# Kernel tuning notes

Measured on AMD Instinct MI355X. Metric: run time of the kernel, lower is better.

Reference implementation:

```python
import jax, jax.numpy as jnp
import numpy as np
from jax import lax

D_MODEL = 128
D_INNER = 256   # expand * d_model
D_STATE = 16
D_CONV = 4
DT_RANK = 8     # ceil(d_model / 16)
IN_CH = 64
SCALE = 0.02


def setup_inputs() -> dict:
    key = jax.random.key(0)
    ks = jax.random.split(key, 16)
    r = lambda k, s: jax.random.normal(k, s, dtype=jnp.float32)
    return {
        "x": r(ks[0], (4, IN_CH, 128, 128)),
        "conv_w": r(ks[1], (D_MODEL, IN_CH, 3, 3)) * SCALE,
        "conv_b": r(ks[2], (D_MODEL,)) * SCALE,
        "bn_g": jnp.ones((D_MODEL,), jnp.float32),
        "bn_b": jnp.zeros((D_MODEL,), jnp.float32),
        "bn_mean": r(ks[3], (D_MODEL,)) * SCALE,
        "bn_var": jax.random.uniform(ks[4], (D_MODEL,), jnp.float32) + 0.5,
        "in_w": r(ks[5], (2 * D_INNER, D_MODEL)) * SCALE,
        "conv1d_w": r(ks[6], (D_INNER, 1, D_CONV)) * SCALE,
        "conv1d_b": r(ks[7], (D_INNER,)) * SCALE,
        "xproj_w": r(ks[8], (DT_RANK + 2 * D_STATE, D_INNER)) * SCALE,
        "dtproj_w": r(ks[9], (D_INNER, DT_RANK)) * SCALE,
        "dtproj_b": r(ks[10], (D_INNER,)) * SCALE,
        "A_log": r(ks[11], (D_INNER, D_STATE)) * 0.5,
        "Dp": r(ks[12], (D_INNER,)) * SCALE,
        "out_w": r(ks[13], (D_MODEL, D_INNER)) * SCALE,
    }


def _mamba(u, in_w, conv1d_w, conv1d_b, xproj_w, dtproj_w, dtproj_b, A_log, Dp, out_w):
    # u: [B, L, d_model]
    xz = jnp.einsum("bld,ed->ble", u, in_w)          # [B, L, 2*d_inner]
    x_in, z = jnp.split(xz, 2, axis=-1)
    # depthwise causal conv1d over L
    xc = lax.conv_general_dilated(
        x_in.transpose(0, 2, 1), conv1d_w, (1,), [(D_CONV - 1, 0)],
        dimension_numbers=("NCL", "OIL", "NCL"), feature_group_count=D_INNER,
    ) + conv1d_b[None, :, None]
    x_in = jax.nn.silu(xc).transpose(0, 2, 1)         # [B, L, d_inner]

    x_dbl = jnp.einsum("bld,ed->ble", x_in, xproj_w)  # [B, L, dt_rank+2*d_state]
    dt, Bm, Cm = jnp.split(x_dbl, [DT_RANK, DT_RANK + D_STATE], axis=-1)
    delta = jax.nn.softplus(jnp.einsum("blr,dr->bld", dt, dtproj_w) + dtproj_b)

    A = -jnp.exp(A_log)                               # [d_inner, d_state]
    deltaA = jnp.exp(jnp.einsum("bld,dn->bldn", delta, A))        # [B,L,d,n]
    deltaBu = jnp.einsum("bld,bln,bld->bldn", delta, Bm, x_in)    # [B,L,d,n]

    def step(h, inp):
        dA, dBu, c = inp                              # [B,d,n],[B,d,n],[B,n]
        h = dA * h + dBu
        y = jnp.einsum("bdn,bn->bd", h, c)
        return h, y

    Bsz, L = u.shape[0], u.shape[1]
    h0 = jnp.zeros((Bsz, D_INNER, D_STATE), u.dtype)
    _, ys = lax.scan(step, h0, (deltaA.transpose(1, 0, 2, 3),
                                deltaBu.transpose(1, 0, 2, 3),
                                Cm.transpose(1, 0, 2)))
    y = ys.transpose(1, 0, 2) + x_in * Dp             # [B, L, d_inner]
    y = y * jax.nn.silu(z)
    return jnp.einsum("bld,ed->ble", y, out_w)        # [B, L, d_model]


def reference(x, conv_w, conv_b, bn_g, bn_b, bn_mean, bn_var, in_w, conv1d_w,
              conv1d_b, xproj_w, dtproj_w, dtproj_b, A_log, Dp, out_w):
    # downsample: conv3x3 stride2 + BN(eval) + exact GELU
    y = lax.conv_general_dilated(x, conv_w, (2, 2), [(1, 1), (1, 1)],
                                 dimension_numbers=("NCHW", "OIHW", "NCHW"))
    y = y + conv_b[None, :, None, None]
    inv = bn_g / jnp.sqrt(bn_var + 1e-5)
    y = (y - bn_mean[None, :, None, None]) * inv[None, :, None, None] + bn_b[None, :, None, None]
    y = jax.nn.gelu(y, approximate=False)             # [B, C, H, W]

    B, C, H, W = y.shape
    u = y.reshape(B, C, H * W).transpose(0, 2, 1)     # [B, L, C]
    out = _mamba(u, in_w, conv1d_w, conv1d_b, xproj_w, dtproj_w, dtproj_b,
                 A_log, Dp, out_w)
    out = out.transpose(0, 2, 1).reshape(B, C, H, W)
    return y + out
```

## Files before the change

### kernel.cpp

```cpp
#include <hip/hip_runtime.h>
#include <math.h>

#define NB 4
#define LTOK 4096
#define DM 128
#define DI 256
#define NCH 256
#define TCH 16
#define GSZ 16
#define NG  16

#define OFF_A2     0u
#define OFF_BIAS2  73728u
#define OFF_YDSR   84096u
#define OFF_XPRE   2181248u
#define OFF_Z      6375552u
#define OFF_DELTA  10569856u
#define OFF_YABF   12667008u
#define OFF_BC     14764160u
#define OFF_DSUM   15288448u
#define OFF_GS     15550592u
#define OFF_GD     15812736u
#define OFF_XT     15829120u
#define OFF_WBF    17926272u
#define OFF_WCMP   17963136u
#define OFF_YDSBF  18004096u
#define OFF_INWBF  19052672u
#define OFF_OUTWBF 19085440u

#define DEV __device__ __forceinline__
#define L2E 1.4426950408889634f

typedef short bh8 __attribute__((ext_vector_type(8)));
typedef float f4v __attribute__((ext_vector_type(4)));

DEV float fast_silu(float v) {
  return v * __builtin_amdgcn_rcpf(1.f + __expf(-v));
}

DEV unsigned short f2bf(float f) {
  unsigned int u = __float_as_uint(f);
  u = (u + 0x7FFFu + ((u >> 16) & 1u)) >> 16;
  return (unsigned short)u;
}

DEV float bf2f(unsigned short us) {
  return __uint_as_float((unsigned int)us << 16);
}

__global__ __launch_bounds__(256) void k0_prep(
    const float* __restrict__ conv_w, const float* __restrict__ conv_b,
    const float* __restrict__ bn_g, const float* __restrict__ bn_b,
    const float* __restrict__ bn_mean, const float* __restrict__ bn_var,
    const float* __restrict__ xproj_w, const float* __restrict__ A_log,
    const float* __restrict__ dtw, const float* __restrict__ in_w,
    const float* __restrict__ out_w, float* __restrict__ ws) {
  int i = blockIdx.x * 256 + threadIdx.x;
  if (i < 73728) {
    int ci = i & 63; int tap = (i >> 6) % 9; int co = i / 576;
    float inv = bn_g[co] * rsqrtf(bn_var[co] + 1e-5f);
    ((unsigned short*)(ws + OFF_WBF))[i] = f2bf(conv_w[co * 576 + ci * 9 + tap] * inv);
  } else if (i < 73856) {
    int co = i - 73728;
    float inv = bn_g[co] * rsqrtf(bn_var[co] + 1e-5f);
    ws[OFF_BIAS2 + co] = (conv_b[co] - bn_mean[co]) * inv + bn_b[co];
  } else if (i < 77952) {
    int j = i - 73856;
    ws[OFF_A2 + j] = -__expf(A_log[j]) * L2E;
  } else if (i < 159872) {
    int j = i - 77952;
    int n = j >> 8, k = j & 255;
    float v = 0.f;
    if (n < 256) {
#pragma unroll
      for (int r = 0; r < 8; ++r)
        v = fmaf(dtw[n * 8 + r], xproj_w[r * 256 + k], v);
    } else if (n < 288) {
      v = xproj_w[(8 + n - 256) * 256 + k];
    }
    ((unsigned short*)(ws + OFF_WCMP))[j] = f2bf(v);
  } else if (i < 225408) {
    int j = i - 159872;
    ((unsigned short*)(ws + OFF_INWBF))[j] = f2bf(in_w[j]);
  } else if (i < 258176) {
    int j = i - 225408;
    ((unsigned short*)(ws + OFF_OUTWBF))[j] = f2bf(out_w[j]);
  }
}

__global__ __launch_bounds__(256) void k0b_transpose(
    const float* __restrict__ x, unsigned short* __restrict__ xt) {
  __shared__ float t[64][65];
  const int tid = threadIdx.x;
  const int ixh = blockIdx.x & 1;
  const int iy = (blockIdx.x >> 1) & 127;
  const int b = blockIdx.x >> 8;
  {
    const int ixl = tid & 63, cw = tid >> 6;
#pragma unroll 4
    for (int i = 0; i < 16; ++i) {
      int ci = cw * 16 + i;
      t[ci][ixl] = x[(((size_t)(b * 64 + ci) * 128) + iy) * 128 + ixh * 64 + ixl];
    }
  }
  __syncthreads();
  {
    const int cil = tid & 63, iw = tid >> 6;
    unsigned short* dst = xt + (((size_t)(b * 128 + iy) * 128) + ixh * 64) * 64;
#pragma unroll 4
    for (int i = 0; i < 16; ++i) {
      int ix = iw * 16 + i;
      dst[ix * 64 + cil] = f2bf(t[cil][ix]);
    }
  }
}

__global__ __launch_bounds__(256) void k1_conv_mfma(
    const unsigned short* __restrict__ xt, const unsigned short* __restrict__ wbf,
    const float* __restrict__ bias2, unsigned short* __restrict__ ydsr,
    unsigned short* __restrict__ ydsbf) {
  __shared__ unsigned short ldt[64][66];
  const int tid = threadIdx.x;
  const int lane = tid & 63;
  const int w = tid >> 6;
  const int col = lane & 15, quad = lane >> 4;
  const int cohalf = blockIdx.x & 1;
  const int oy = (blockIdx.x >> 1) & 63;
  const int b = blockIdx.x >> 7;
  const int co0 = cohalf * 64 + (w & 1) * 32;
  const int tok0 = (w >> 1) * 32;
  const int iy0 = 2 * oy - 1;
  const bh8 bzero = {};
  f4v acc[2][2];
#pragma unroll
  for (int mt = 0; mt < 2; ++mt)
#pragma unroll
    for (int nt = 0; nt < 2; ++nt) acc[mt][nt] = (f4v){0.f, 0.f, 0.f, 0.f};

  const unsigned short* ap0 = wbf + (size_t)(co0 + col) * 576;
  const unsigned short* ap1 = wbf + (size_t)(co0 + 16 + col) * 576;

  for (int tap = 0; tap < 9; ++tap) {
    const int kh = tap / 3, kw = tap - kh * 3;
    const int iy = iy0 + kh;
    const int ix0 = 2 * (tok0 + col) - 1 + kw;
    const int ix1 = ix0 + 32;
    const unsigned short* xrow = xt + (long)(b * 128 + iy) * 8192;
    const bool ok0 = (iy >= 0) && (ix0 >= 0);
    const bool ok1 = (iy >= 0);
#pragma unroll
    for (int kc = 0; kc < 2; ++kc) {
      const int cib = kc * 32 + quad * 8;
      bh8 a0 = *(const bh8*)&ap0[tap * 64 + cib];
      bh8 a1 = *(const bh8*)&ap1[tap * 64 + cib];
      bh8 b0 = *(const bh8*)&xrow[(long)ix0 * 64 + cib];
      bh8 b1 = *(const bh8*)&xrow[(long)ix1 * 64 + cib];
      if (!ok0) b0 = bzero;
      if (!ok1) b1 = bzero;
      acc[0][0] = __builtin_amdgcn_mfma_f32_16x16x32_bf16(a0, b0, acc[0][0], 0, 0, 0);
      acc[1][0] = __builtin_amdgcn_mfma_f32_16x16x32_bf16(a1, b0, acc[1][0], 0, 0, 0);
      acc[0][1] = __builtin_amdgcn_mfma_f32_16x16x32_bf16(a0, b1, acc[0][1], 0, 0, 0);
      acc[1][1] = __builtin_amdgcn_mfma_f32_16x16x32_bf16(a1, b1, acc[1][1], 0, 0, 0);
    }
  }
#pragma unroll
  for (int mt = 0; mt < 2; ++mt)
#pragma unroll
    for (int nt = 0; nt < 2; ++nt) {
      const int tok = tok0 + nt * 16 + col;
#pragma unroll
      for (int r = 0; r < 4; ++r) {
        const int co = co0 + mt * 16 + quad * 4 + r;
        float v = acc[mt][nt][r] + bias2[co];
        float g = 0.5f * v * (1.f + erff(v * 0.70710678118f));
        unsigned short gb = f2bf(g);
        ydsr[(((size_t)(b * 128 + co) * 64) + oy) * 64 + tok] = gb;
        ldt[tok][(w & 1) * 32 + mt * 16 + quad * 4 + r] = gb;
      }
    }
  __syncthreads();
  {
    const int tok = tid >> 2, cg = (tid & 3) * 16;
    unsigned short* dst =
        ydsbf + ((size_t)(b * 4096 + oy * 64 + tok)) * 128 + cohalf * 64 + cg;
#pragma unroll
    for (int j = 0; j < 8; ++j)
      ((unsigned int*)dst)[j] = *(const unsigned int*)&ldt[tok][cg + 2 * j];
  }
}

__global__ __launch_bounds__(256) void k2_mfma(
    const unsigned short* __restrict__ ydsbf, const unsigned short* __restrict__ inwbf,
    unsigned short* __restrict__ xpre, unsigned short* __restrict__ z) {
  const int tid = threadIdx.x;
  const int lane = tid & 63;
  const int w = tid >> 6;
  const int col = lane & 15, quad = lane >> 4;
  const int tt = blockIdx.x & 255, b = blockIdx.x >> 8;
  const int t0 = tt * 16;
  bh8 afrag[4];
  {
    const unsigned short* arow = ydsbf + (size_t)(b * 4096 + t0 + col) * 128 + quad * 8;
#pragma unroll
    for (int kb = 0; kb < 4; ++kb) afrag[kb] = *(const bh8*)&arow[kb * 32];
  }
  f4v acc[8];
#pragma unroll
  for (int j = 0; j < 8; ++j) acc[j] = (f4v){0.f, 0.f, 0.f, 0.f};
  const int nt0 = w * 8;
  const unsigned short* wb = inwbf + (size_t)(nt0 * 16 + col) * 128 + quad * 8;
#pragma unroll
  for (int kb = 0; kb < 4; ++kb) {
#pragma unroll
    for (int j = 0; j < 8; ++j) {
      bh8 bfrag = *(const bh8*)&wb[(size_t)j * 2048 + kb * 32];
      acc[j] = __builtin_amdgcn_mfma_f32_16x16x32_bf16(afrag[kb], bfrag, acc[j], 0, 0, 0);
    }
  }
#pragma unroll
  for (int j = 0; j < 8; ++j) {
    const int e = (nt0 + j) * 16 + col;
#pragma unroll
    for (int r = 0; r < 4; ++r) {
      const int t = t0 + quad * 4 + r;
      if (e < 256) xpre[((size_t)(b * 4096 + t)) * 256 + e] = f2bf(acc[j][r]);
      else z[((size_t)(b * 4096 + t)) * 256 + e - 256] = f2bf(acc[j][r]);
    }
  }
}

__global__ __launch_bounds__(256) void k4_mfma(
    const unsigned short* __restrict__ wcomp, const float* __restrict__ dtb,
    const unsigned short* __restrict__ xpre, const float* __restrict__ cw1,
    const float* __restrict__ cb1, unsigned short* __restrict__ xinbf,
    unsigned short* __restrict__ delta, float* __restrict__ bc,
    float* __restrict__ dsum) {
  __shared__ unsigned short ld_xin[16][264];
  __shared__ unsigned short ld_delta[16][264];
  __shared__ float ld_bc[16][33];
  const int tid = threadIdx.x;
  const int lane = tid & 63;
  const int w = tid >> 6;
  const int col = lane & 15, quad = lane >> 4;
  const int tt = blockIdx.x & 255, b = blockIdx.x >> 8;
  const int t0 = tt * 16;

  {
    const int d = tid;
    float4 w4 = *(const float4*)&cw1[d * 4];
    float bias = cb1[d];
    float xw[19];
#pragma unroll
    for (int i = 0; i < 19; ++i) {
      int t = t0 - 3 + i;
      xw[i] = (t >= 0) ? bf2f(xpre[((size_t)(b * 4096 + t)) * 256 + d]) : 0.f;
    }
    unsigned short* dst = xinbf + ((size_t)(b * 4096 + t0)) * 256 + d;
#pragma unroll
    for (int i = 0; i < 16; ++i) {
      float o = bias + w4.x * xw[i] + w4.y * xw[i + 1] + w4.z * xw[i + 2] +
                w4.w * xw[i + 3];
      unsigned short us = f2bf(fast_silu(o));
      ld_xin[i][d] = us;
      dst[(size_t)i * 256] = us;
    }
  }
  __syncthreads();

  bh8 afrag[8];
#pragma unroll
  for (int kb = 0; kb < 8; ++kb)
    afrag[kb] = *(const bh8*)&ld_xin[col][quad * 8 + kb * 32];
  f4v acc[5];
#pragma unroll
  for (int j = 0; j < 5; ++j) acc[j] = (f4v){0.f, 0.f, 0.f, 0.f};

  const int nt0 = w * 5;
  const unsigned short* wb = wcomp + (size_t)(nt0 * 16 + col) * 256 + quad * 8;
#pragma unroll
  for (int kb = 0; kb < 8; ++kb) {
#pragma unroll
    for (int j = 0; j < 5; ++j) {
      bh8 bfrag = *(const bh8*)&wb[(size_t)j * 4096 + kb * 32];
      acc[j] = __builtin_amdgcn_mfma_f32_16x16x32_bf16(afrag[kb], bfrag, acc[j], 0, 0, 0);
    }
  }
#pragma unroll
  for (int j = 0; j < 5; ++j) {
    const int n = (nt0 + j) * 16 + col;
    if (n < 256) {
      float bias = dtb[n];
#pragma unroll
      for (int r = 0; r < 4; ++r) {
        float s = acc[j][r] + bias;
        float dl = fmaxf(s, 0.f) + __logf(1.f + __expf(-fabsf(s)));
        ld_delta[quad * 4 + r][n] = f2bf(dl);
      }
    } else if (n < 288) {
#pragma unroll
      for (int r = 0; r < 4; ++r) ld_bc[quad * 4 + r][n - 256] = acc[j][r];
    }
  }
  __syncthreads();

  {
    float ds = 0.f;
#pragma unroll
    for (int i = 0; i < 16; ++i) ds += bf2f(ld_delta[i][tid]);
    dsum[((size_t)b * 256 + tt) * 256 + tid] = ds;
  }
#pragma unroll
  for (int it = 0; it < 4; ++it) {
    int idx = it * 256 + tid;
    int row = idx >> 6, d4 = (idx & 63) * 4;
    unsigned long long pk = *(const unsigned long long*)&ld_delta[row][d4];
    *(unsigned long long*)&delta[((size_t)(b * 4096 + t0 + row)) * 256 + d4] = pk;
  }
  if (tid < 128) {
    int row = tid >> 3, q = (tid & 7) * 4;
    float4 v = make_float4(ld_bc[row][q], ld_bc[row][q + 1],
                           ld_bc[row][q + 2], ld_bc[row][q + 3]);
    *(float4*)&bc[((size_t)(b * 4096 + t0 + row)) * 32 + q] = v;
  }
}

__global__ __launch_bounds__(256) void k5a_scan1(
    const unsigned short* __restrict__ xinbf, const float* __restrict__ bc,
    const unsigned short* __restrict__ delta, const float* __restrict__ a2tab,
    float* __restrict__ S) {
  __shared__ __align__(16) float bct[TCH * 32];
  const int tid = threadIdx.x;
  const int d = tid;
  const int c = blockIdx.x & (NCH - 1), b = blockIdx.x >> 8;
  const int t0 = c * TCH;
  {
    const float* src = bc + (size_t)(b * 4096 + t0) * 32;
    for (int i = tid; i < TCH * 32; i += 256) bct[i] = src[i];
  }
  float A2[16];
#pragma unroll
  for (int j = 0; j < 4; ++j) {
    float4 a = *(const float4*)&a2tab[d * 16 + j * 4];
    A2[4 * j + 0] = a.x; A2[4 * j + 1] = a.y; A2[4 * j + 2] = a.z; A2[4 * j + 3] = a.w;
  }
  float h[16];
#pragma unroll
  for (int n = 0; n < 16; ++n) h[n] = 0.f;
  const unsigned short* pd = delta + (size_t)(b * 4096 + t0) * 256 + d;
  const unsigned short* px = xinbf + (size_t)(b * 4096 + t0) * 256 + d;
  __syncthreads();
#pragma unroll 4
  for (int i = 0; i < TCH; ++i) {
    float dl = bf2f(pd[(size_t)i * 256]);
    float xv = bf2f(px[(size_t)i * 256]);
    float dlx = dl * xv;
    const float* r = &bct[i * 32];
    float4 B0 = *(const float4*)&r[0];
    float4 B1 = *(const float4*)&r[4];
    float4 B2 = *(const float4*)&r[8];
    float4 B3 = *(const float4*)&r[12];
    float Bv[16] = {B0.x, B0.y, B0.z, B0.w, B1.x, B1.y, B1.z, B1.w,
                    B2.x, B2.y, B2.z, B2.w, B3.x, B3.y, B3.z, B3.w};
#pragma unroll
    for (int n = 0; n < 16; ++n)
      h[n] = fmaf(exp2f(dl * A2[n]), h[n], dlx * Bv[n]);
  }
  const size_t sbase = ((size_t)(b * NCH + c) * 16) * 256 + d;
#pragma unroll
  for (int n = 0; n < 16; ++n) S[sbase + (size_t)n * 256] = h[n];
}

__global__ __launch_bounds__(256) void k5b1_group(
    float* __restrict__ S, const float* __restrict__ dsum,
    const float* __restrict__ a2tab, float* __restrict__ Gs,
    float* __restrict__ Gd) {
  const int d = threadIdx.x;
  const int n = blockIdx.x & 15, g = (blockIdx.x >> 4) & (NG - 1),
            b = blockIdx.x >> 8;
  const float A2 = a2tab[d * 16 + n];
  float h = 0.f, cum = 0.f;
#pragma unroll 4
  for (int c16 = 0; c16 < GSZ; ++c16) {
    int c = g * GSZ + c16;
    size_t si = ((size_t)(b * NCH + c) * 16 + n) * 256 + d;
    float s = S[si];
    float dsv = dsum[((size_t)b * NCH + c) * 256 + d];
    float P = exp2f(A2 * dsv);
    S[si] = h;
    h = fmaf(P, h, s);
    cum += dsv;
  }
  Gs[((size_t)(b * NG + g) * 16 + n) * 256 + d] = h;
  if (n == 0) Gd[((size_t)b * NG + g) * 256 + d] = cum;
}

__global__ __launch_bounds__(256) void k5b2_groupscan(
    float* __restrict__ Gs, const float* __restrict__ Gd,
    const float* __restrict__ a2tab) {
  const int d = threadIdx.x;
  const int n = blockIdx.x & 15, b = blockIdx.x >> 4;
  const float A2 = a2tab[d * 16 + n];
  float h = 0.f;
#pragma unroll
  for (int g = 0; g < NG; ++g) {
    size_t gi = ((size_t)(b * NG + g) * 16 + n) * 256 + d;
    float s = Gs[gi];
    float P = exp2f(A2 * Gd[((size_t)b * NG + g) * 256 + d]);
    Gs[gi] = h;
    h = fmaf(P, h, s);
  }
}

__global__ __launch_bounds__(256) void k5c_scan2(
    const unsigned short* __restrict__ xinbf, const float* __restrict__ bc,
    const unsigned short* __restrict__ delta, const unsigned short* __restrict__ z,
    const float* __restrict__ a2tab, const float* __restrict__ Dp,
    const float* __restrict__ dsum, const float* __restrict__ Gs,
    const float* __restrict__ S, unsigned short* __restrict__ yabf) {
  __shared__ __align__(16) float bct[TCH * 32];
  const int tid = threadIdx.x;
  const int d = tid;
  const int c = blockIdx.x & (NCH - 1), b = blockIdx.x >> 8;
  const int t0 = c * TCH;
  {
    const float* src = bc + (size_t)(b * 4096 + t0) * 32;
    for (int i = tid; i < TCH * 32; i += 256) bct[i] = src[i];
  }
  float A2[16];
#pragma unroll
  for (int j = 0; j < 4; ++j) {
    float4 a = *(const float4*)&a2tab[d * 16 + j * 4];
    A2[4 * j + 0] = a.x; A2[4 * j + 1] = a.y; A2[4 * j + 2] = a.z; A2[4 * j + 3] = a.w;
  }
  const float Dpd = Dp[d];
  const int g = c >> 4, c16 = c & 15;
  float dpref = 0.f;
  {
    const float* pds = dsum + ((size_t)b * NCH + g * GSZ) * 256 + d;
    for (int cc = 0; cc < c16; ++cc) dpref += pds[(size_t)cc * 256];
  }
  const size_t sbase = ((size_t)(b * NCH + c) * 16) * 256 + d;
  const size_t gbase = ((size_t)(b * NG + g) * 16) * 256 + d;
  float h[16];
#pragma unroll
  for (int n = 0; n < 16; ++n) {
    float gi = Gs[gbase + (size_t)n * 256];
    float hl = S[sbase + (size_t)n * 256];
    h[n] = fmaf(exp2f(A2[n] * dpref), gi, hl);
  }
  const size_t base = (size_t)(b * 4096 + t0) * 256 + d;
  const unsigned short* pd = delta + base;
  const unsigned short* px = xinbf + base;
  const unsigned short* pz = z + base;
  unsigned short* py = yabf + base;
  __syncthreads();
#pragma unroll 4
  for (int i = 0; i < TCH; ++i) {
    float dl = bf2f(pd[(size_t)i * 256]);
    float xv = bf2f(px[(size_t)i * 256]);
    float zv = bf2f(pz[(size_t)i * 256]);
    float dlx = dl * xv;
    const float* r = &bct[i * 32];
    float4 B0 = *(const float4*)&r[0];
    float4 B1 = *(const float4*)&r[4];
    float4 B2 = *(const float4*)&r[8];
    float4 B3 = *(const float4*)&r[12];
    float4 C0 = *(const float4*)&r[16];
    float4 C1 = *(const float4*)&r[20];
    float4 C2 = *(const float4*)&r[24];
    float4 C3 = *(const float4*)&r[28];
    float Bv[16] = {B0.x, B0.y, B0.z, B0.w, B1.x, B1.y, B1.z, B1.w,
                    B2.x, B2.y, B2.z, B2.w, B3.x, B3.y, B3.z, B3.w};
    float Cv[16] = {C0.x, C0.y, C0.z, C0.w, C1.x, C1.y, C1.z, C1.w,
                    C2.x, C2.y, C2.z, C2.w, C3.x, C3.y, C3.z, C3.w};
    float y = 0.f;
#pragma unroll
    for (int n = 0; n < 16; ++n) {
      h[n] = fmaf(exp2f(dl * A2[n]), h[n], dlx * Bv[n]);
      y = fmaf(h[n], Cv[n], y);
    }
    py[(size_t)i * 256] = f2bf((y + xv * Dpd) * fast_silu(zv));
  }
}

__global__ __launch_bounds__(256) void k6_mfma(
    const unsigned short* __restrict__ yabf, const unsigned short* __restrict__ outwbf,
    const unsigned short* __restrict__ ydsr, float* __restrict__ out) {
  __shared__ float ld[16][132];
  const int tid = threadIdx.x;
  const int lane = tid & 63;
  const int w = tid >> 6;
  const int col = lane & 15, quad = lane >> 4;
  const int tt = blockIdx.x & 255, b = blockIdx.x >> 8;
  const int t0 = tt * 16;
  const int oy = t0 >> 6, ox0 = t0 & 63;
  bh8 afrag[8];
  {
    const unsigned short* arow = yabf + (size_t)(b * 4096 + t0 + col) * 256 + quad * 8;
#pragma unroll
    for (int kb = 0; kb < 8; ++kb) afrag[kb] = *(const bh8*)&arow[kb * 32];
  }
  f4v acc[2];
#pragma unroll
  for (int j = 0; j < 2; ++j) acc[j] = (f4v){0.f, 0.f, 0.f, 0.f};
  const int nt0 = w * 2;
  const unsigned short* wb = outwbf + (size_t)(nt0 * 16 + col) * 256 + quad * 8;
#pragma unroll
  for (int kb = 0; kb < 8; ++kb) {
#pragma unroll
    for (int j = 0; j < 2; ++j) {
      bh8 bfrag = *(const bh8*)&wb[(size_t)j * 4096 + kb * 32];
      acc[j] = __builtin_amdgcn_mfma_f32_16x16x32_bf16(afrag[kb], bfrag, acc[j], 0, 0, 0);
    }
  }
#pragma unroll
  for (int j = 0; j < 2; ++j)
#pragma unroll
    for (int r = 0; r < 4; ++r)
      ld[quad * 4 + r][(nt0 + j) * 16 + col] = acc[j][r];
  __syncthreads();
  {
    const int cc = tid >> 1, half = tid & 1;
    size_t base = (((size_t)(b * 128 + cc) * 64) + oy) * 64 + ox0 + half * 8;
    const unsigned short* rp = ydsr + base;
    const int m0 = half * 8;
    float4 o0 = make_float4(ld[m0 + 0][cc] + bf2f(rp[0]), ld[m0 + 1][cc] + bf2f(rp[1]),
                            ld[m0 + 2][cc] + bf2f(rp[2]), ld[m0 + 3][cc] + bf2f(rp[3]));
    float4 o1 = make_float4(ld[m0 + 4][cc] + bf2f(rp[4]), ld[m0 + 5][cc] + bf2f(rp[5]),
                            ld[m0 + 6][cc] + bf2f(rp[6]), ld[m0 + 7][cc] + bf2f(rp[7]));
    *(float4*)&out[base] = o0;
    *(float4*)&out[base + 4] = o1;
  }
}

extern "C" void kernel_launch(void* const* d_in, const int* in_sizes, int n_in,
                              void* d_out, int out_size, void* d_ws, size_t ws_size,
                              hipStream_t stream) {
  (void)in_sizes; (void)n_in; (void)out_size; (void)ws_size;
  const float* x        = (const float*)d_in[0];
  const float* conv_w   = (const float*)d_in[1];
  const float* conv_b   = (const float*)d_in[2];
  const float* bn_g     = (const float*)d_in[3];
  const float* bn_b     = (const float*)d_in[4];
  const float* bn_mean  = (const float*)d_in[5];
  const float* bn_var   = (const float*)d_in[6];
  const float* in_w     = (const float*)d_in[7];
  const float* conv1d_w = (const float*)d_in[8];
  const float* conv1d_b = (const float*)d_in[9];
  const float* xproj_w  = (const float*)d_in[10];
  const float* dtproj_w = (const float*)d_in[11];
  const float* dtproj_b = (const float*)d_in[12];
  const float* A_log    = (const float*)d_in[13];
  const float* Dp       = (const float*)d_in[14];
  const float* out_w    = (const float*)d_in[15];
  float* ws = (float*)d_ws;
  float* out = (float*)d_out;

  k0_prep<<<1009, 256, 0, stream>>>(conv_w, conv_b, bn_g, bn_b, bn_mean, bn_var,
                                    xproj_w, A_log, dtproj_w, in_w, out_w, ws);
  k0b_transpose<<<1024, 256, 0, stream>>>(x, (unsigned short*)(ws + OFF_XT));
  k1_conv_mfma<<<512, 256, 0, stream>>>((const unsigned short*)(ws + OFF_XT),
                                        (const unsigned short*)(ws + OFF_WBF),
                                        ws + OFF_BIAS2,
                                        (unsigned short*)(ws + OFF_YDSR),
                                        (unsigned short*)(ws + OFF_YDSBF));
  k2_mfma<<<1024, 256, 0, stream>>>((const unsigned short*)(ws + OFF_YDSBF),
                                    (const unsigned short*)(ws + OFF_INWBF),
                                    (unsigned short*)(ws + OFF_XPRE),
                                    (unsigned short*)(ws + OFF_Z));
  k4_mfma<<<1024, 256, 0, stream>>>((const unsigned short*)(ws + OFF_WCMP),
                                    dtproj_b,
                                    (const unsigned short*)(ws + OFF_XPRE),
                                    conv1d_w, conv1d_b,
                                    (unsigned short*)(ws + OFF_XT),
                                    (unsigned short*)(ws + OFF_DELTA),
                                    ws + OFF_BC, ws + OFF_DSUM);
  k5a_scan1<<<1024, 256, 0, stream>>>((const unsigned short*)(ws + OFF_XT),
                                      ws + OFF_BC,
                                      (const unsigned short*)(ws + OFF_DELTA),
                                      ws + OFF_A2, ws + OFF_XPRE);
  k5b1_group<<<1024, 256, 0, stream>>>(ws + OFF_XPRE, ws + OFF_DSUM, ws + OFF_A2,
                                       ws + OFF_GS, ws + OFF_GD);
  k5b2_groupscan<<<64, 256, 0, stream>>>(ws + OFF_GS, ws + OFF_GD, ws + OFF_A2);
  k5c_scan2<<<1024, 256, 0, stream>>>((const unsigned short*)(ws + OFF_XT),
                                      ws + OFF_BC,
                                      (const unsigned short*)(ws + OFF_DELTA),
                                      (const unsigned short*)(ws + OFF_Z),
                                      ws + OFF_A2, Dp, ws + OFF_DSUM,
                                      ws + OFF_GS, ws + OFF_XPRE,
                                      (unsigned short*)(ws + OFF_YABF));
  k6_mfma<<<1024, 256, 0, stream>>>((const unsigned short*)(ws + OFF_YABF),
                                    (const unsigned short*)(ws + OFF_OUTWBF),
                                    (const unsigned short*)(ws + OFF_YDSR), out);
}
```

Before: 240.9 us.

## Fuse chunked scan phases into one cooperative kernel with grid syncs

```diff
diff --git a/kernel.cpp b/kernel.cpp
--- a/kernel.cpp
+++ b/kernel.cpp
@@ -1,5 +1,8 @@
 #include <hip/hip_runtime.h>
+#include <hip/hip_cooperative_groups.h>
 #include <math.h>
+
+namespace cg = cooperative_groups;
 
 #define NB 4
 #define LTOK 4096
@@ -27,6 +30,7 @@
 #define OFF_YDSBF  18004096u
 #define OFF_INWBF  19052672u
 #define OFF_OUTWBF 19085440u
+#define OFF_DPREF  19101824u
 
 #define DEV __device__ __forceinline__
 #define L2E 1.4426950408889634f
@@ -48,14 +52,42 @@
   return __uint_as_float((unsigned int)us << 16);
 }
 
-__global__ __launch_bounds__(256) void k0_prep(
-    const float* __restrict__ conv_w, const float* __restrict__ conv_b,
-    const float* __restrict__ bn_g, const float* __restrict__ bn_b,
-    const float* __restrict__ bn_mean, const float* __restrict__ bn_var,
-    const float* __restrict__ xproj_w, const float* __restrict__ A_log,
-    const float* __restrict__ dtw, const float* __restrict__ in_w,
-    const float* __restrict__ out_w, float* __restrict__ ws) {
-  int i = blockIdx.x * 256 + threadIdx.x;
+__global__ __launch_bounds__(256) void k0_all(
+    const float* __restrict__ x, const float* __restrict__ conv_w,
+    const float* __restrict__ conv_b, const float* __restrict__ bn_g,
+    const float* __restrict__ bn_b, const float* __restrict__ bn_mean,
+    const float* __restrict__ bn_var, const float* __restrict__ xproj_w,
+    const float* __restrict__ A_log, const float* __restrict__ dtw,
+    const float* __restrict__ in_w, const float* __restrict__ out_w,
+    float* __restrict__ ws) {
+  const int tid = threadIdx.x;
+  if (blockIdx.x < 1024) {
+    __shared__ float t[64][65];
+    unsigned short* xt = (unsigned short*)(ws + OFF_XT);
+    const int ixh = blockIdx.x & 1;
+    const int iy = (blockIdx.x >> 1) & 127;
+    const int b = blockIdx.x >> 8;
+    {
+      const int ixl = tid & 63, cw = tid >> 6;
+#pragma unroll 4
+      for (int i = 0; i < 16; ++i) {
+        int ci = cw * 16 + i;
+        t[ci][ixl] = x[(((size_t)(b * 64 + ci) * 128) + iy) * 128 + ixh * 64 + ixl];
+      }
+    }
+    __syncthreads();
+    {
+      const int cil = tid & 63, iw = tid >> 6;
+      unsigned short* dst = xt + (((size_t)(b * 128 + iy) * 128) + ixh * 64) * 64;
+#pragma unroll 4
+      for (int i = 0; i < 16; ++i) {
+        int ix = iw * 16 + i;
+        dst[ix * 64 + cil] = f2bf(t[cil][ix]);
+      }
+    }
+    return;
+  }
+  int i = (blockIdx.x - 1024) * 256 + tid;
   if (i < 73728) {
     int ci = i & 63; int tap = (i >> 6) % 9; int co = i / 576;
     float inv = bn_g[co] * rsqrtf(bn_var[co] + 1e-5f);
@@ -85,33 +117,6 @@
   } else if (i < 258176) {
     int j = i - 225408;
     ((unsigned short*)(ws + OFF_OUTWBF))[j] = f2bf(out_w[j]);
-  }
-}
-
-__global__ __launch_bounds__(256) void k0b_transpose(
-    const float* __restrict__ x, unsigned short* __restrict__ xt) {
-  __shared__ float t[64][65];
-  const int tid = threadIdx.x;
-  const int ixh = blockIdx.x & 1;
-  const int iy = (blockIdx.x >> 1) & 127;
-  const int b = blockIdx.x >> 8;
-  {
-    const int ixl = tid & 63, cw = tid >> 6;
-#pragma unroll 4
-    for (int i = 0; i < 16; ++i) {
-      int ci = cw * 16 + i;
-      t[ci][ixl] = x[(((size_t)(b * 64 + ci) * 128) + iy) * 128 + ixh * 64 + ixl];
-    }
-  }
-  __syncthreads();
-  {
-    const int cil = tid & 63, iw = tid >> 6;
-    unsigned short* dst = xt + (((size_t)(b * 128 + iy) * 128) + ixh * 64) * 64;
-#pragma unroll 4
-    for (int i = 0; i < 16; ++i) {
-      int ix = iw * 16 + i;
-      dst[ix * 64 + cil] = f2bf(t[cil][ix]);
-    }
   }
 }
 
@@ -180,12 +185,12 @@
     }
   __syncthreads();
   {
-    const int tok = tid >> 2, cg = (tid & 3) * 16;
+    const int tok = tid >> 2, cg2 = (tid & 3) * 16;
     unsigned short* dst =
-        ydsbf + ((size_t)(b * 4096 + oy * 64 + tok)) * 128 + cohalf * 64 + cg;
+        ydsbf + ((size_t)(b * 4096 + oy * 64 + tok)) * 128 + cohalf * 64 + cg2;
 #pragma unroll
     for (int j = 0; j < 8; ++j)
-      ((unsigned int*)dst)[j] = *(const unsigned int*)&ldt[tok][cg + 2 * j];
+      ((unsigned int*)dst)[j] = *(const unsigned int*)&ldt[tok][cg2 + 2 * j];
   }
 }
 
@@ -233,8 +238,7 @@
     const unsigned short* __restrict__ wcomp, const float* __restrict__ dtb,
     const unsigned short* __restrict__ xpre, const float* __restrict__ cw1,
     const float* __restrict__ cb1, unsigned short* __restrict__ xinbf,
-    unsigned short* __restrict__ delta, float* __restrict__ bc,
-    float* __restrict__ dsum) {
+    unsigned short* __restrict__ delta, float* __restrict__ bc) {
   __shared__ unsigned short ld_xin[16][264];
   __shared__ unsigned short ld_delta[16][264];
   __shared__ float ld_bc[16][33];
@@ -303,12 +307,6 @@
   }
   __syncthreads();
 
-  {
-    float ds = 0.f;
-#pragma unroll
-    for (int i = 0; i < 16; ++i) ds += bf2f(ld_delta[i][tid]);
-    dsum[((size_t)b * 256 + tt) * 256 + tid] = ds;
-  }
 #pragma unroll
   for (int it = 0; it < 4; ++it) {
     int idx = it * 256 + tid;
@@ -324,14 +322,18 @@
   }
 }
 
-__global__ __launch_bounds__(256) void k5a_scan1(
+__global__ __launch_bounds__(256, 4) void kscan_fused(
     const unsigned short* __restrict__ xinbf, const float* __restrict__ bc,
-    const unsigned short* __restrict__ delta, const float* __restrict__ a2tab,
-    float* __restrict__ S) {
+    const unsigned short* __restrict__ delta, const unsigned short* __restrict__ z,
+    const float* __restrict__ a2tab, const float* __restrict__ Dp,
+    unsigned short* S, float* dsum, float* dpref, float* Gs, float* Gd,
+    unsigned short* __restrict__ yabf) {
+  cg::grid_group grid = cg::this_grid();
   __shared__ __align__(16) float bct[TCH * 32];
   const int tid = threadIdx.x;
   const int d = tid;
-  const int c = blockIdx.x & (NCH - 1), b = blockIdx.x >> 8;
+  const int bx = blockIdx.x;
+  const int c = bx & 255, b = bx >> 8;
   const int t0 = c * TCH;
   {
     const float* src = bc + (size_t)(b * 4096 + t0) * 32;
@@ -343,143 +345,118 @@
     float4 a = *(const float4*)&a2tab[d * 16 + j * 4];
     A2[4 * j + 0] = a.x; A2[4 * j + 1] = a.y; A2[4 * j + 2] = a.z; A2[4 * j + 3] = a.w;
   }
-  float h[16];
-#pragma unroll
-  for (int n = 0; n < 16; ++n) h[n] = 0.f;
-  const unsigned short* pd = delta + (size_t)(b * 4096 + t0) * 256 + d;
-  const unsigned short* px = xinbf + (size_t)(b * 4096 + t0) * 256 + d;
+  float dl[16], xv[16];
+  {
+    const unsigned short* pd = delta + (size_t)(b * 4096 + t0) * 256 + d;
+    const unsigned short* px = xinbf + (size_t)(b * 4096 + t0) * 256 + d;
+#pragma unroll
+    for (int i = 0; i < TCH; ++i) {
+      dl[i] = bf2f(pd[(size_t)i * 256]);
+      xv[i] = bf2f(px[(size_t)i * 256]);
+    }
+  }
   __syncthreads();
+  const size_t sbase = ((size_t)(b * NCH + c) * 16) * 256 + d;
+  {
+    float h[16];
+#pragma unroll
+    for (int n = 0; n < 16; ++n) h[n] = 0.f;
+    float ds = 0.f;
 #pragma unroll 4
-  for (int i = 0; i < TCH; ++i) {
-    float dl = bf2f(pd[(size_t)i * 256]);
-    float xv = bf2f(px[(size_t)i * 256]);
-    float dlx = dl * xv;
-    const float* r = &bct[i * 32];
-    float4 B0 = *(const float4*)&r[0];
-    float4 B1 = *(const float4*)&r[4];
-    float4 B2 = *(const float4*)&r[8];
-    float4 B3 = *(const float4*)&r[12];
-    float Bv[16] = {B0.x, B0.y, B0.z, B0.w, B1.x, B1.y, B1.z, B1.w,
-                    B2.x, B2.y, B2.z, B2.w, B3.x, B3.y, B3.z, B3.w};
-#pragma unroll
-    for (int n = 0; n < 16; ++n)
-      h[n] = fmaf(exp2f(dl * A2[n]), h[n], dlx * Bv[n]);
-  }
-  const size_t sbase = ((size_t)(b * NCH + c) * 16) * 256 + d;
-#pragma unroll
-  for (int n = 0; n < 16; ++n) S[sbase + (size_t)n * 256] = h[n];
-}
-
-__global__ __launch_bounds__(256) void k5b1_group(
-    float* __restrict__ S, const float* __restrict__ dsum,
-    const float* __restrict__ a2tab, float* __restrict__ Gs,
-    float* __restrict__ Gd) {
-  const int d = threadIdx.x;
-  const int n = blockIdx.x & 15, g = (blockIdx.x >> 4) & (NG - 1),
-            b = blockIdx.x >> 8;
-  const float A2 = a2tab[d * 16 + n];
-  float h = 0.f, cum = 0.f;
+    for (int i = 0; i < TCH; ++i) {
+      float dlx = dl[i] * xv[i];
+      ds += dl[i];
+      const float* r = &bct[i * 32];
+      float4 B0 = *(const float4*)&r[0];
+      float4 B1 = *(const float4*)&r[4];
+      float4 B2 = *(const float4*)&r[8];
+      float4 B3 = *(const float4*)&r[12];
+      float Bv[16] = {B0.x, B0.y, B0.z, B0.w, B1.x, B1.y, B1.z, B1.w,
+                      B2.x, B2.y, B2.z, B2.w, B3.x, B3.y, B3.z, B3.w};
+#pragma unroll
+      for (int n = 0; n < 16; ++n)
+        h[n] = fmaf(exp2f(dl[i] * A2[n]), h[n], dlx * Bv[n]);
+    }
+#pragma unroll
+    for (int n = 0; n < 16; ++n) S[sbase + (size_t)n * 256] = f2bf(h[n]);
+    dsum[((size_t)b * NCH + c) * 256 + d] = ds;
+  }
+  __threadfence();
+  grid.sync();
+  {
+    const int n = bx & 15, g = (bx >> 4) & 15, bb = bx >> 8;
+    const float A2v = a2tab[d * 16 + n];
+    float h = 0.f, cum = 0.f;
 #pragma unroll 4
-  for (int c16 = 0; c16 < GSZ; ++c16) {
-    int c = g * GSZ + c16;
-    size_t si = ((size_t)(b * NCH + c) * 16 + n) * 256 + d;
-    float s = S[si];
-    float dsv = dsum[((size_t)b * NCH + c) * 256 + d];
-    float P = exp2f(A2 * dsv);
-    S[si] = h;
-    h = fmaf(P, h, s);
-    cum += dsv;
-  }
-  Gs[((size_t)(b * NG + g) * 16 + n) * 256 + d] = h;
-  if (n == 0) Gd[((size_t)b * NG + g) * 256 + d] = cum;
-}
-
-__global__ __launch_bounds__(256) void k5b2_groupscan(
-    float* __restrict__ Gs, const float* __restrict__ Gd,
-    const float* __restrict__ a2tab) {
-  const int d = threadIdx.x;
-  const int n = blockIdx.x & 15, b = blockIdx.x >> 4;
-  const float A2 = a2tab[d * 16 + n];
-  float h = 0.f;
-#pragma unroll
-  for (int g = 0; g < NG; ++g) {
-    size_t gi = ((size_t)(b * NG + g) * 16 + n) * 256 + d;
-    float s = Gs[gi];
-    float P = exp2f(A2 * Gd[((size_t)b * NG + g) * 256 + d]);
-    Gs[gi] = h;
-    h = fmaf(P, h, s);
-  }
-}
-
-__global__ __launch_bounds__(256) void k5c_scan2(
-    const unsigned short* __restrict__ xinbf, const float* __restrict__ bc,
-    const unsigned short* __restrict__ delta, const unsigned short* __restrict__ z,
-    const float* __restrict__ a2tab, const float* __restrict__ Dp,
-    const float* __restrict__ dsum, const float* __restrict__ Gs,
-    const float* __restrict__ S, unsigned short* __restrict__ yabf) {
-  __shared__ __align__(16) float bct[TCH * 32];
-  const int tid = threadIdx.x;
-  const int d = tid;
-  const int c = blockIdx.x & (NCH - 1), b = blockIdx.x >> 8;
-  const int t0 = c * TCH;
-  {
-    const float* src = bc + (size_t)(b * 4096 + t0) * 32;
-    for (int i = tid; i < TCH * 32; i += 256) bct[i] = src[i];
-  }
-  float A2[16];
-#pragma unroll
-  for (int j = 0; j < 4; ++j) {
-    float4 a = *(const float4*)&a2tab[d * 16 + j * 4];
-    A2[4 * j + 0] = a.x; A2[4 * j + 1] = a.y; A2[4 * j + 2] = a.z; A2[4 * j + 3] = a.w;
-  }
-  const float Dpd = Dp[d];
-  const int g = c >> 4, c16 = c & 15;
-  float dpref = 0.f;
-  {
-    const float* pds = dsum + ((size_t)b * NCH + g * GSZ) * 256 + d;
-    for (int cc = 0; cc < c16; ++cc) dpref += pds[(size_t)cc * 256];
-  }
-  const size_t sbase = ((size_t)(b * NCH + c) * 16) * 256 + d;
-  const size_t gbase = ((size_t)(b * NG + g) * 16) * 256 + d;
-  float h[16];
-#pragma unroll
-  for (int n = 0; n < 16; ++n) {
-    float gi = Gs[gbase + (size_t)n * 256];
-    float hl = S[sbase + (size_t)n * 256];
-    h[n] = fmaf(exp2f(A2[n] * dpref), gi, hl);
-  }
-  const size_t base = (size_t)(b * 4096 + t0) * 256 + d;
-  const unsigned short* pd = delta + base;
-  const unsigned short* px = xinbf + base;
-  const unsigned short* pz = z + base;
-  unsigned short* py = yabf + base;
-  __syncthreads();
+    for (int c16 = 0; c16 < GSZ; ++c16) {
+      int cc = g * GSZ + c16;
+      size_t si = ((size_t)(bb * NCH + cc) * 16 + n) * 256 + d;
+      float s = bf2f(S[si]);
+      float dsv = dsum[((size_t)bb * NCH + cc) * 256 + d];
+      if (n == 0) dpref[((size_t)bb * NCH + cc) * 256 + d] = cum;
+      S[si] = f2bf(h);
+      h = fmaf(exp2f(A2v * dsv), h, s);
+      cum += dsv;
+    }
+    Gs[((size_t)(bb * NG + g) * 16 + n) * 256 + d] = h;
+    if (n == 0) Gd[((size_t)bb * NG + g) * 256 + d] = cum;
+  }
+  __threadfence();
+  grid.sync();
+  if (bx < 64) {
+    const int n = bx & 15, bb = bx >> 4;
+    const float A2v = a2tab[d * 16 + n];
+    float h = 0.f;
+#pragma unroll
+    for (int g = 0; g < NG; ++g) {
+      size_t gi = ((size_t)(bb * NG + g) * 16 + n) * 256 + d;
+      float s = Gs[gi];
+      float P = exp2f(A2v * Gd[((size_t)bb * NG + g) * 256 + d]);
+      Gs[gi] = h;
+      h = fmaf(P, h, s);
+    }
+  }
+  __threadfence();
+  grid.sync();
+  {
+    const int g = c >> 4;
+    const float Dpd = Dp[d];
+    float dpr = dpref[((size_t)b * NCH + c) * 256 + d];
+    const size_t gbase = ((size_t)(b * NG + g) * 16) * 256 + d;
+    float h[16];
+#pragma unroll
+    for (int n = 0; n < 16; ++n) {
+      float gi = Gs[gbase + (size_t)n * 256];
+      float hl = bf2f(S[sbase + (size_t)n * 256]);
+      h[n] = fmaf(exp2f(A2[n] * dpr), gi, hl);
+    }
+    const unsigned short* pz = z + (size_t)(b * 4096 + t0) * 256 + d;
+    unsigned short* py = yabf + (size_t)(b * 4096 + t0) * 256 + d;
 #pragma unroll 4
-  for (int i = 0; i < TCH; ++i) {
-    float dl = bf2f(pd[(size_t)i * 256]);
-    float xv = bf2f(px[(size_t)i * 256]);
-    float zv = bf2f(pz[(size_t)i * 256]);
-    float dlx = dl * xv;
-    const float* r = &bct[i * 32];
-    float4 B0 = *(const float4*)&r[0];
-    float4 B1 = *(const float4*)&r[4];
-    float4 B2 = *(const float4*)&r[8];
-    float4 B3 = *(const float4*)&r[12];
-    float4 C0 = *(const float4*)&r[16];
-    float4 C1 = *(const float4*)&r[20];
-    float4 C2 = *(const float4*)&r[24];
-    float4 C3 = *(const float4*)&r[28];
-    float Bv[16] = {B0.x, B0.y, B0.z, B0.w, B1.x, B1.y, B1.z, B1.w,
-                    B2.x, B2.y, B2.z, B2.w, B3.x, B3.y, B3.z, B3.w};
-    float Cv[16] = {C0.x, C0.y, C0.z, C0.w, C1.x, C1.y, C1.z, C1.w,
-                    C2.x, C2.y, C2.z, C2.w, C3.x, C3.y, C3.z, C3.w};
-    float y = 0.f;
-#pragma unroll
-    for (int n = 0; n < 16; ++n) {
-      h[n] = fmaf(exp2f(dl * A2[n]), h[n], dlx * Bv[n]);
-      y = fmaf(h[n], Cv[n], y);
-    }
-    py[(size_t)i * 256] = f2bf((y + xv * Dpd) * fast_silu(zv));
+    for (int i = 0; i < TCH; ++i) {
+      float dlx = dl[i] * xv[i];
+      const float* r = &bct[i * 32];
+      float4 B0 = *(const float4*)&r[0];
+      float4 B1 = *(const float4*)&r[4];
+      float4 B2 = *(const float4*)&r[8];
+      float4 B3 = *(const float4*)&r[12];
+      float4 C0 = *(const float4*)&r[16];
+      float4 C1 = *(const float4*)&r[20];
+      float4 C2 = *(const float4*)&r[24];
+      float4 C3 = *(const float4*)&r[28];
+      float Bv[16] = {B0.x, B0.y, B0.z, B0.w, B1.x, B1.y, B1.z, B1.w,
+                      B2.x, B2.y, B2.z, B2.w, B3.x, B3.y, B3.z, B3.w};
+      float Cv[16] = {C0.x, C0.y, C0.z, C0.w, C1.x, C1.y, C1.z, C1.w,
+                      C2.x, C2.y, C2.z, C2.w, C3.x, C3.y, C3.z, C3.w};
+      float y = 0.f;
+#pragma unroll
+      for (int n = 0; n < 16; ++n) {
+        h[n] = fmaf(exp2f(dl[i] * A2[n]), h[n], dlx * Bv[n]);
+        y = fmaf(h[n], Cv[n], y);
+      }
+      float zv = bf2f(pz[(size_t)i * 256]);
+      py[(size_t)i * 256] = f2bf((y + xv[i] * Dpd) * fast_silu(zv));
+    }
   }
 }
 
@@ -556,9 +533,9 @@
   float* ws = (float*)d_ws;
   float* out = (float*)d_out;
 
-  k0_prep<<<1009, 256, 0, stream>>>(conv_w, conv_b, bn_g, bn_b, bn_mean, bn_var,
-                                    xproj_w, A_log, dtproj_w, in_w, out_w, ws);
-  k0b_transpose<<<1024, 256, 0, stream>>>(x, (unsigned short*)(ws + OFF_XT));
+  k0_all<<<2033, 256, 0, stream>>>(x, conv_w, conv_b, bn_g, bn_b, bn_mean,
+                                   bn_var, xproj_w, A_log, dtproj_w, in_w,
+                                   out_w, ws);
   k1_conv_mfma<<<512, 256, 0, stream>>>((const unsigned short*)(ws + OFF_XT),
                                         (const unsigned short*)(ws + OFF_WBF),
                                         ws + OFF_BIAS2,
@@ -574,21 +551,25 @@
                                     conv1d_w, conv1d_b,
                                     (unsigned short*)(ws + OFF_XT),
                                     (unsigned short*)(ws + OFF_DELTA),
-                                    ws + OFF_BC, ws + OFF_DSUM);
-  k5a_scan1<<<1024, 256, 0, stream>>>((const unsigned short*)(ws + OFF_XT),
-                                      ws + OFF_BC,
-                                      (const unsigned short*)(ws + OFF_DELTA),
-                                      ws + OFF_A2, ws + OFF_XPRE);
-  k5b1_group<<<1024, 256, 0, stream>>>(ws + OFF_XPRE, ws + OFF_DSUM, ws + OFF_A2,
-                                       ws + OFF_GS, ws + OFF_GD);
-  k5b2_groupscan<<<64, 256, 0, stream>>>(ws + OFF_GS, ws + OFF_GD, ws + OFF_A2);
-  k5c_scan2<<<1024, 256, 0, stream>>>((const unsigned short*)(ws + OFF_XT),
-                                      ws + OFF_BC,
-                                      (const unsigned short*)(ws + OFF_DELTA),
-                                      (const unsigned short*)(ws + OFF_Z),
-                                      ws + OFF_A2, Dp, ws + OFF_DSUM,
-                                      ws + OFF_GS, ws + OFF_XPRE,
-                                      (unsigned short*)(ws + OFF_YABF));
+                                    ws + OFF_BC);
+  {
+    const unsigned short* xinbf_p = (const unsigned short*)(ws + OFF_XT);
+    const float* bc_p = ws + OFF_BC;
+    const unsigned short* delta_p = (const unsigned short*)(ws + OFF_DELTA);
+    const unsigned short* z_p = (const unsigned short*)(ws + OFF_Z);
+    const float* a2_p = ws + OFF_A2;
+    const float* dp_p = Dp;
+    unsigned short* s_p = (unsigned short*)(ws + OFF_XPRE);
+    float* dsum_p = ws + OFF_DSUM;
+    float* dpref_p = ws + OFF_DPREF;
+    float* gs_p = ws + OFF_GS;
+    float* gd_p = ws + OFF_GD;
+    unsigned short* yabf_p = (unsigned short*)(ws + OFF_YABF);
+    void* args[] = {&xinbf_p, &bc_p, &delta_p, &z_p, &a2_p, &dp_p,
+                    &s_p, &dsum_p, &dpref_p, &gs_p, &gd_p, &yabf_p};
+    hipLaunchCooperativeKernel((void*)kscan_fused, dim3(1024), dim3(256),
+                               args, 0, stream);
+  }
   k6_mfma<<<1024, 256, 0, stream>>>((const unsigned short*)(ws + OFF_YABF),
                                     (const unsigned short*)(ws + OFF_OUTWBF),
                                     (const unsigned short*)(ws + OFF_YDSR), out);
```

New measurement: 819.2 us. +240.0%, slower.

## Merge prep kernels, store chunk states in bf16, precompute per-chunk delta prefix

Applied to the files above, without the earlier changes.

```diff
diff --git a/kernel.cpp b/kernel.cpp
--- a/kernel.cpp
+++ b/kernel.cpp
@@ -27,6 +27,7 @@
 #define OFF_YDSBF  18004096u
 #define OFF_INWBF  19052672u
 #define OFF_OUTWBF 19085440u
+#define OFF_DPREF  19101824u
 
 #define DEV __device__ __forceinline__
 #define L2E 1.4426950408889634f
@@ -48,14 +49,42 @@
   return __uint_as_float((unsigned int)us << 16);
 }
 
-__global__ __launch_bounds__(256) void k0_prep(
-    const float* __restrict__ conv_w, const float* __restrict__ conv_b,
-    const float* __restrict__ bn_g, const float* __restrict__ bn_b,
-    const float* __restrict__ bn_mean, const float* __restrict__ bn_var,
-    const float* __restrict__ xproj_w, const float* __restrict__ A_log,
-    const float* __restrict__ dtw, const float* __restrict__ in_w,
-    const float* __restrict__ out_w, float* __restrict__ ws) {
-  int i = blockIdx.x * 256 + threadIdx.x;
+__global__ __launch_bounds__(256) void k0_all(
+    const float* __restrict__ x, const float* __restrict__ conv_w,
+    const float* __restrict__ conv_b, const float* __restrict__ bn_g,
+    const float* __restrict__ bn_b, const float* __restrict__ bn_mean,
+    const float* __restrict__ bn_var, const float* __restrict__ xproj_w,
+    const float* __restrict__ A_log, const float* __restrict__ dtw,
+    const float* __restrict__ in_w, const float* __restrict__ out_w,
+    float* __restrict__ ws) {
+  const int tid = threadIdx.x;
+  if (blockIdx.x < 1024) {
+    __shared__ float t[64][65];
+    unsigned short* xt = (unsigned short*)(ws + OFF_XT);
+    const int ixh = blockIdx.x & 1;
+    const int iy = (blockIdx.x >> 1) & 127;
+    const int b = blockIdx.x >> 8;
+    {
+      const int ixl = tid & 63, cw = tid >> 6;
+#pragma unroll 4
+      for (int i = 0; i < 16; ++i) {
+        int ci = cw * 16 + i;
+        t[ci][ixl] = x[(((size_t)(b * 64 + ci) * 128) + iy) * 128 + ixh * 64 + ixl];
+      }
+    }
+    __syncthreads();
+    {
+      const int cil = tid & 63, iw = tid >> 6;
+      unsigned short* dst = xt + (((size_t)(b * 128 + iy) * 128) + ixh * 64) * 64;
+#pragma unroll 4
+      for (int i = 0; i < 16; ++i) {
+        int ix = iw * 16 + i;
+        dst[ix * 64 + cil] = f2bf(t[cil][ix]);
+      }
+    }
+    return;
+  }
+  int i = (blockIdx.x - 1024) * 256 + tid;
   if (i < 73728) {
     int ci = i & 63; int tap = (i >> 6) % 9; int co = i / 576;
     float inv = bn_g[co] * rsqrtf(bn_var[co] + 1e-5f);
@@ -88,33 +117,6 @@
   }
 }
 
-__global__ __launch_bounds__(256) void k0b_transpose(
-    const float* __restrict__ x, unsigned short* __restrict__ xt) {
-  __shared__ float t[64][65];
-  const int tid = threadIdx.x;
-  const int ixh = blockIdx.x & 1;
-  const int iy = (blockIdx.x >> 1) & 127;
-  const int b = blockIdx.x >> 8;
-  {
-    const int ixl = tid & 63, cw = tid >> 6;
-#pragma unroll 4
-    for (int i = 0; i < 16; ++i) {
-      int ci = cw * 16 + i;
-      t[ci][ixl] = x[(((size_t)(b * 64 + ci) * 128) + iy) * 128 + ixh * 64 + ixl];
-    }
-  }
-  __syncthreads();
-  {
-    const int cil = tid & 63, iw = tid >> 6;
-    unsigned short* dst = xt + (((size_t)(b * 128 + iy) * 128) + ixh * 64) * 64;
-#pragma unroll 4
-    for (int i = 0; i < 16; ++i) {
-      int ix = iw * 16 + i;
-      dst[ix * 64 + cil] = f2bf(t[cil][ix]);
-    }
-  }
-}
-
 __global__ __launch_bounds__(256) void k1_conv_mfma(
     const unsigned short* __restrict__ xt, const unsigned short* __restrict__ wbf,
     const float* __restrict__ bias2, unsigned short* __restrict__ ydsr,
@@ -180,12 +182,12 @@
     }
   __syncthreads();
   {
-    const int tok = tid >> 2, cg = (tid & 3) * 16;
+    const int tok = tid >> 2, cg2 = (tid & 3) * 16;
     unsigned short* dst =
-        ydsbf + ((size_t)(b * 4096 + oy * 64 + tok)) * 128 + cohalf * 64 + cg;
+        ydsbf + ((size_t)(b * 4096 + oy * 64 + tok)) * 128 + cohalf * 64 + cg2;
 #pragma unroll
     for (int j = 0; j < 8; ++j)
-      ((unsigned int*)dst)[j] = *(const unsigned int*)&ldt[tok][cg + 2 * j];
+      ((unsigned int*)dst)[j] = *(const unsigned int*)&ldt[tok][cg2 + 2 * j];
   }
 }
 
@@ -233,8 +235,7 @@
     const unsigned short* __restrict__ wcomp, const float* __restrict__ dtb,
     const unsigned short* __restrict__ xpre, const float* __restrict__ cw1,
     const float* __restrict__ cb1, unsigned short* __restrict__ xinbf,
-    unsigned short* __restrict__ delta, float* __restrict__ bc,
-    float* __restrict__ dsum) {
+    unsigned short* __restrict__ delta, float* __restrict__ bc) {
   __shared__ unsigned short ld_xin[16][264];
   __shared__ unsigned short ld_delta[16][264];
   __shared__ float ld_bc[16][33];
@@ -303,12 +304,6 @@
   }
   __syncthreads();
 
-  {
-    float ds = 0.f;
-#pragma unroll
-    for (int i = 0; i < 16; ++i) ds += bf2f(ld_delta[i][tid]);
-    dsum[((size_t)b * 256 + tt) * 256 + tid] = ds;
-  }
 #pragma unroll
   for (int it = 0; it < 4; ++it) {
     int idx = it * 256 + tid;
@@ -327,7 +322,7 @@
 __global__ __launch_bounds__(256) void k5a_scan1(
     const unsigned short* __restrict__ xinbf, const float* __restrict__ bc,
     const unsigned short* __restrict__ delta, const float* __restrict__ a2tab,
-    float* __restrict__ S) {
+    unsigned short* __restrict__ S, float* __restrict__ dsum) {
   __shared__ __align__(16) float bct[TCH * 32];
   const int tid = threadIdx.x;
   const int d = tid;
@@ -346,6 +341,7 @@
   float h[16];
 #pragma unroll
   for (int n = 0; n < 16; ++n) h[n] = 0.f;
+  float ds = 0.f;
   const unsigned short* pd = delta + (size_t)(b * 4096 + t0) * 256 + d;
   const unsigned short* px = xinbf + (size_t)(b * 4096 + t0) * 256 + d;
   __syncthreads();
@@ -354,6 +350,7 @@
     float dl = bf2f(pd[(size_t)i * 256]);
     float xv = bf2f(px[(size_t)i * 256]);
     float dlx = dl * xv;
+    ds += dl;
     const float* r = &bct[i * 32];
     float4 B0 = *(const float4*)&r[0];
     float4 B1 = *(const float4*)&r[4];
@@ -367,13 +364,14 @@
   }
   const size_t sbase = ((size_t)(b * NCH + c) * 16) * 256 + d;
 #pragma unroll
-  for (int n = 0; n < 16; ++n) S[sbase + (size_t)n * 256] = h[n];
+  for (int n = 0; n < 16; ++n) S[sbase + (size_t)n * 256] = f2bf(h[n]);
+  dsum[((size_t)b * NCH + c) * 256 + d] = ds;
 }
 
 __global__ __launch_bounds__(256) void k5b1_group(
-    float* __restrict__ S, const float* __restrict__ dsum,
-    const float* __restrict__ a2tab, float* __restrict__ Gs,
-    float* __restrict__ Gd) {
+    unsigned short* __restrict__ S, const float* __restrict__ dsum,
+    const float* __restrict__ a2tab, float* __restrict__ dpref,
+    float* __restrict__ Gs, float* __restrict__ Gd) {
   const int d = threadIdx.x;
   const int n = blockIdx.x & 15, g = (blockIdx.x >> 4) & (NG - 1),
             b = blockIdx.x >> 8;
@@ -383,11 +381,11 @@
   for (int c16 = 0; c16 < GSZ; ++c16) {
     int c = g * GSZ + c16;
     size_t si = ((size_t)(b * NCH + c) * 16 + n) * 256 + d;
-    float s = S[si];
+    float s = bf2f(S[si]);
     float dsv = dsum[((size_t)b * NCH + c) * 256 + d];
-    float P = exp2f(A2 * dsv);
-    S[si] = h;
-    h = fmaf(P, h, s);
+    if (n == 0) dpref[((size_t)b * NCH + c) * 256 + d] = cum;
+    S[si] = f2bf(h);
+    h = fmaf(exp2f(A2 * dsv), h, s);
     cum += dsv;
   }
   Gs[((size_t)(b * NG + g) * 16 + n) * 256 + d] = h;
@@ -415,8 +413,8 @@
     const unsigned short* __restrict__ xinbf, const float* __restrict__ bc,
     const unsigned short* __restrict__ delta, const unsigned short* __restrict__ z,
     const float* __restrict__ a2tab, const float* __restrict__ Dp,
-    const float* __restrict__ dsum, const float* __restrict__ Gs,
-    const float* __restrict__ S, unsigned short* __restrict__ yabf) {
+    const float* __restrict__ dpref, const float* __restrict__ Gs,
+    const unsigned short* __restrict__ S, unsigned short* __restrict__ yabf) {
   __shared__ __align__(16) float bct[TCH * 32];
   const int tid = threadIdx.x;
   const int d = tid;
@@ -433,20 +431,16 @@
     A2[4 * j + 0] = a.x; A2[4 * j + 1] = a.y; A2[4 * j + 2] = a.z; A2[4 * j + 3] = a.w;
   }
   const float Dpd = Dp[d];
-  const int g = c >> 4, c16 = c & 15;
-  float dpref = 0.f;
-  {
-    const float* pds = dsum + ((size_t)b * NCH + g * GSZ) * 256 + d;
-    for (int cc = 0; cc < c16; ++cc) dpref += pds[(size_t)cc * 256];
-  }
+  const int g = c >> 4;
+  const float dpr = dpref[((size_t)b * NCH + c) * 256 + d];
   const size_t sbase = ((size_t)(b * NCH + c) * 16) * 256 + d;
   const size_t gbase = ((size_t)(b * NG + g) * 16) * 256 + d;
   float h[16];
 #pragma unroll
   for (int n = 0; n < 16; ++n) {
     float gi = Gs[gbase + (size_t)n * 256];
-    float hl = S[sbase + (size_t)n * 256];
-    h[n] = fmaf(exp2f(A2[n] * dpref), gi, hl);
+    float hl = bf2f(S[sbase + (size_t)n * 256]);
+    h[n] = fmaf(exp2f(A2[n] * dpr), gi, hl);
   }
   const size_t base = (size_t)(b * 4096 + t0) * 256 + d;
   const unsigned short* pd = delta + base;
@@ -556,9 +550,9 @@
   float* ws = (float*)d_ws;
   float* out = (float*)d_out;
 
-  k0_prep<<<1009, 256, 0, stream>>>(conv_w, conv_b, bn_g, bn_b, bn_mean, bn_var,
-                                    xproj_w, A_log, dtproj_w, in_w, out_w, ws);
-  k0b_transpose<<<1024, 256, 0, stream>>>(x, (unsigned short*)(ws + OFF_XT));
+  k0_all<<<2033, 256, 0, stream>>>(x, conv_w, conv_b, bn_g, bn_b, bn_mean,
+                                   bn_var, xproj_w, A_log, dtproj_w, in_w,
+                                   out_w, ws);
   k1_conv_mfma<<<512, 256, 0, stream>>>((const unsigned short*)(ws + OFF_XT),
                                         (const unsigned short*)(ws + OFF_WBF),
                                         ws + OFF_BIAS2,
@@ -574,20 +568,24 @@
                                     conv1d_w, conv1d_b,
                                     (unsigned short*)(ws + OFF_XT),
                                     (unsigned short*)(ws + OFF_DELTA),
-                                    ws + OFF_BC, ws + OFF_DSUM);
+                                    ws + OFF_BC);
   k5a_scan1<<<1024, 256, 0, stream>>>((const unsigned short*)(ws + OFF_XT),
                                       ws + OFF_BC,
                                       (const unsigned short*)(ws + OFF_DELTA),
-                                      ws + OFF_A2, ws + OFF_XPRE);
-  k5b1_group<<<1024, 256, 0, stream>>>(ws + OFF_XPRE, ws + OFF_DSUM, ws + OFF_A2,
-                                       ws + OFF_GS, ws + OFF_GD);
+                                      ws + OFF_A2,
+                                      (unsigned short*)(ws + OFF_XPRE),
+                                      ws + OFF_DSUM);
+  k5b1_group<<<1024, 256, 0, stream>>>((unsigned short*)(ws + OFF_XPRE),
+                                       ws + OFF_DSUM, ws + OFF_A2,
+                                       ws + OFF_DPREF, ws + OFF_GS, ws + OFF_GD);
   k5b2_groupscan<<<64, 256, 0, stream>>>(ws + OFF_GS, ws + OFF_GD, ws + OFF_A2);
   k5c_scan2<<<1024, 256, 0, stream>>>((const unsigned short*)(ws + OFF_XT),
                                       ws + OFF_BC,
                                       (const unsigned short*)(ws + OFF_DELTA),
                                       (const unsigned short*)(ws + OFF_Z),
-                                      ws + OFF_A2, Dp, ws + OFF_DSUM,
-                                      ws + OFF_GS, ws + OFF_XPRE,
+                                      ws + OFF_A2, Dp, ws + OFF_DPREF,
+                                      ws + OFF_GS,
+                                      (const unsigned short*)(ws + OFF_XPRE),
                                       (unsigned short*)(ws + OFF_YABF));
   k6_mfma<<<1024, 256, 0, stream>>>((const unsigned short*)(ws + OFF_YABF),
                                     (const unsigned short*)(ws + OFF_OUTWBF),
```

Measured after the change: 241.9 us. About the same (+0.4%).
